# Kernel optimization log

Measured on AMD Instinct MI355X. Metric: run time of the kernel, lower is better.

The kernel has to match this reference:

```python
import jax, jax.numpy as jnp
import numpy as np

B, T, H, N, D, L, V = 4, 1024, 4, 4096, 256, 6, 256
Dh = N // H  # per-head dim; RoPE max_pos == Dh so T <= Dh
EPS = 1e-5


def _ln(x):
    # LayerNorm over last dim, no affine, eps=1e-5 (torch default)
    m = jnp.mean(x, axis=-1, keepdims=True)
    v = jnp.mean((x - m) ** 2, axis=-1, keepdims=True)
    return (x - m) / jnp.sqrt(v + EPS)


def _rope_tables(seq_len, head_dim):
    inv_freq = 1.0 / (10000.0 ** (jnp.arange(0, head_dim, 2, dtype=jnp.float32) / head_dim))
    t = jnp.arange(seq_len, dtype=jnp.float32)
    freqs = jnp.outer(t, inv_freq)            # [T, Dh/2]
    emb = jnp.concatenate([freqs, freqs], -1)  # [T, Dh]
    return jnp.cos(emb), jnp.sin(emb)


def _rotate_half(x):
    d = x.shape[-1]
    return jnp.concatenate([-x[..., d // 2:], x[..., :d // 2]], axis=-1)


def setup_inputs() -> dict:
    key = jax.random.key(0)
    ks = jax.random.split(key, 6)
    tokens = jax.random.randint(ks[0], (B, T), 0, V)
    emb_w = 0.02 * jax.random.normal(ks[1], (V, D), dtype=jnp.float32)
    E = 0.02 * jax.random.normal(ks[2], (N, D), dtype=jnp.float32)
    Dx = 0.02 * jax.random.normal(ks[3], (H, D, Dh), dtype=jnp.float32)
    Dy = 0.02 * jax.random.normal(ks[4], (H, D, Dh), dtype=jnp.float32)
    readout = 0.02 * jax.random.normal(ks[5], (D, V), dtype=jnp.float32)
    return {"tokens": tokens, "emb_w": emb_w, "E": E, "Dx": Dx, "Dy": Dy, "readout": readout}


def reference(tokens, emb_w, E, Dx, Dy, readout):
    b, t = tokens.shape
    dh = Dx.shape[-1]
    cos, sin = _rope_tables(t, dh)  # [T, Dh], broadcast over B,H
    v = _ln(emb_w[tokens])          # [B, T, D]
    for _ in range(L):
        x = jax.nn.relu(jnp.einsum('btd,hde->bhte', v, Dx))       # [B,H,T,Dh]
        xr = x * cos + _rotate_half(x) * sin                       # RoPE (Q and K share)
        scores = jnp.einsum('bhte,bhse->bhts', xr, xr)             # [B,H,T,T] (no softmax)
        a = jnp.einsum('bhts,bsd->bhtd', scores, v)                # [B,H,T,D]
        y = jax.nn.relu(jnp.einsum('bhtd,hde->bhte', a, Dy)) * x   # [B,H,T,Dh]
        y = jnp.transpose(y, (0, 2, 1, 3)).reshape(b, t, -1)       # [B,T,N]
        v = _ln(v + _ln(y @ E))
    return v @ readout  # [B,T,V]
```

## Files before the change

kernel.cpp:

```cpp
#include <hip/hip_runtime.h>
#include <cstdint>

namespace {

typedef _Float16 f16_t;
typedef _Float16 f16x8 __attribute__((ext_vector_type(8)));
typedef float    f32x4 __attribute__((ext_vector_type(4)));
typedef float    f32x16 __attribute__((ext_vector_type(16)));

constexpr int Bc = 4, Tc = 1024, Hc = 4, Dc = 256, DHc = 1024, Lc = 6, Vc = 256;
constexpr int HALFc = 512;
constexpr float EPS = 1e-5f;
constexpr long long T4q  = (long long)Tc * 4096;
constexpr long long TDq  = (long long)Tc * Dc;
constexpr long long HDDq = (long long)DHc * Dc;
constexpr long long TBUFq = (long long)Bc * Tc * Dc;

__device__ __forceinline__ int pe_perm(int v) {
  return (v & ~1023) | ((v & 511) << 1) | ((v >> 9) & 1);
}

__device__ __forceinline__ void gload16(const void* g, void* l) {
  __builtin_amdgcn_global_load_lds((const __attribute__((address_space(1))) void*)g,
                                   (__attribute__((address_space(3))) void*)l, 16, 0, 0);
}


template<int NW>
__device__ __forceinline__ void stage_kmaj(const f16_t* __restrict__ P, int k0,
                                           int ld, int c0, f16_t* S, int tid) {
  const int cg  = tid & 15;
  const int kpb = tid >> 4;
  constexpr int NP = (NW == 4) ? 2 : 1;
  #pragma unroll
  for (int p = 0; p < NP; ++p) {
    const int kp = p * 16 + kpb;
    const int k  = kp * 2;
    const f16x8 r0 = *(const f16x8*)(P + (size_t)(k0 + k) * ld + c0 + cg * 8);
    const f16x8 r1 = *(const f16x8*)(P + (size_t)(k0 + k + 1) * ld + c0 + cg * 8);
    #pragma unroll
    for (int j = 0; j < 8; ++j) {
      const int n = cg * 8 + j;
      union { f16_t h[2]; unsigned int u; } pk;
      pk.h[0] = r0[j]; pk.h[1] = r1[j];
      ((unsigned int*)S)[n * 32 + ((((kp >> 2) ^ (n & 7) ^ ((n >> 3) & 7)) & 7) << 2)
                         + (kp & 3)] = pk.u;
    }
  }
}

template<int EPI, bool AKMAJ, bool BKMAJ, int NW>
__global__ __launch_bounds__(NW * 64)
void gemm_f16(const f16_t* __restrict__ A, long long sAb, long long sAh,
              const f16_t* __restrict__ B, long long sBb, long long sBh,
              void* __restrict__ Cv, long long sCb, long long sCh,
              const f16_t* __restrict__ aux,
              int K, int lda, int ldb, int ldc,
              const float* __restrict__ cosP, const float* __restrict__ sinP)
{
  constexpr int FN2  = (NW == 4) ? 2 : 1;
  constexpr int WCW  = FN2 * 32;
  constexpr int NTHR = NW * 64;
  constexpr int SP   = 1024 / NTHR;
  constexpr int RPP  = NTHR / 8;

  __shared__ __align__(16) f16_t As[128 * 64];
  __shared__ __align__(16) f16_t Bs[128 * 64];

  const int zb = blockIdx.z >> 2, zh = blockIdx.z & 3;
  A += zb * sAb + zh * sAh;
  B += zb * sBb + zh * sBh;
  const long long Coff = zb * sCb + zh * sCh;

  const int tid  = threadIdx.x;
  const int lane = tid & 63;
  const int wave = tid >> 6;
  const int wr = (NW == 4) ? (wave >> 1) : (wave >> 2);
  const int wc = (NW == 4) ? (wave & 1)  : (wave & 3);
  const int m0 = blockIdx.y * 128, n0 = blockIdx.x * 128;

  const int lrow  = tid >> 3;
  const int lslot = tid & 7;

  f32x16 acc[2][FN2] = {};

  for (int k0 = 0; k0 < K; k0 += 64) {
    if (!AKMAJ) {
      #pragma unroll
      for (int c = 0; c < SP; ++c) {
        const int row  = c * RPP + lrow;
        const int scol = ((lslot ^ (row & 7) ^ ((row >> 3) & 7)) << 3);
        gload16(A + (size_t)(m0 + row) * lda + k0 + scol, &As[(c * NTHR + tid) * 8]);
      }
    } else {
      stage_kmaj<NW>(A, k0, lda, m0, As, tid);
    }
    if (!BKMAJ) {
      #pragma unroll
      for (int c = 0; c < SP; ++c) {
        const int row  = c * RPP + lrow;
        const int scol = ((lslot ^ (row & 7) ^ ((row >> 3) & 7)) << 3);
        gload16(B + (size_t)(n0 + row) * ldb + k0 + scol, &Bs[(c * NTHR + tid) * 8]);
      }
    } else {
      stage_kmaj<NW>(B, k0, ldb, n0, Bs, tid);
    }
    __syncthreads();

    #pragma unroll
    for (int kc = 0; kc < 4; ++kc) {
      f16x8 af[2], bf[FN2];
      #pragma unroll
      for (int m = 0; m < 2; ++m) {
        const int r  = wr * 64 + m * 32 + (lane & 31);
        const int sl = (kc * 2 + (lane >> 5)) ^ (r & 7) ^ ((r >> 3) & 7);
        af[m] = *(const f16x8*)(&As[r * 64 + sl * 8]);
      }
      #pragma unroll
      for (int n = 0; n < FN2; ++n) {
        const int r  = wc * WCW + n * 32 + (lane & 31);
        const int sl = (kc * 2 + (lane >> 5)) ^ (r & 7) ^ ((r >> 3) & 7);
        bf[n] = *(const f16x8*)(&Bs[r * 64 + sl * 8]);
      }
      #pragma unroll
      for (int m = 0; m < 2; ++m)
        #pragma unroll
        for (int n = 0; n < FN2; ++n)
          acc[m][n] = __builtin_amdgcn_mfma_f32_32x32x16_f16(af[m], bf[n], acc[m][n], 0, 0, 0);
    }
    __syncthreads();
  }

  const int rbase = 4 * (lane >> 5);
  if (EPI == 4) {
    float* C = (float*)Cv + Coff;
    #pragma unroll
    for (int m = 0; m < 2; ++m)
      #pragma unroll
      for (int n = 0; n < FN2; ++n) {
        const int gcol = n0 + wc * WCW + n * 32 + (lane & 31);
        #pragma unroll
        for (int reg = 0; reg < 16; ++reg) {
          const int grow = m0 + wr * 64 + m * 32 + (reg & 3) + 8 * (reg >> 2) + rbase;
          C[(long long)grow * ldc + gcol] = acc[m][n][reg];
        }
      }
  } else if (EPI == 5) {
    f16_t* C = (f16_t*)Cv + Coff;
    #pragma unroll
    for (int m = 0; m < 2; ++m)
      #pragma unroll
      for (int n = 0; n < FN2; ++n) {
        const int gcol = n0 + wc * WCW + n * 32 + (lane & 31);
        const int jj   = (gcol & 1023) >> 1;
        const float sg = (gcol & 1) ? 1.0f : -1.0f;
        #pragma unroll
        for (int reg = 0; reg < 16; ++reg) {
          const int grow = m0 + wr * 64 + m * 32 + (reg & 3) + 8 * (reg >> 2) + rbase;
          const int tt   = grow & (Tc - 1);
          const float val  = fmaxf(acc[m][n][reg], 0.0f);
          const float part = __shfl_xor(val, 1);
          const float c = cosP[tt * HALFc + jj];
          const float s = sinP[tt * HALFc + jj];
          C[(long long)grow * ldc + gcol] = (f16_t)(val * c + part * s * sg);
        }
      }
  } else if (EPI == 2) {
    f16_t* C = (f16_t*)Cv + Coff;
    const f16_t* X = aux + Coff;
    #pragma unroll
    for (int m = 0; m < 2; ++m)
      #pragma unroll
      for (int n = 0; n < FN2; ++n) {
        const int gcol = n0 + wc * WCW + n * 32 + (lane & 31);
        const int jj   = (gcol & 1023) >> 1;
        const float sg = (gcol & 1) ? 1.0f : -1.0f;
        #pragma unroll
        for (int reg = 0; reg < 16; ++reg) {
          const int grow = m0 + wr * 64 + m * 32 + (reg & 3) + 8 * (reg >> 2) + rbase;
          const int tt   = grow & (Tc - 1);
          const long long off = (long long)grow * ldc + gcol;
          const float xrv  = (float)X[off];
          const float part = __shfl_xor(xrv, 1);
          const float c = cosP[tt * HALFc + jj];
          const float s = sinP[tt * HALFc + jj];
          const float xv = xrv * c - part * s * sg;
          C[off] = (f16_t)(fmaxf(acc[m][n][reg], 0.0f) * xv);
        }
      }
  } else {
    f16_t* C = (f16_t*)Cv + Coff;
    #pragma unroll
    for (int m = 0; m < 2; ++m)
      #pragma unroll
      for (int n = 0; n < FN2; ++n) {
        const int gcol = n0 + wc * WCW + n * 32 + (lane & 31);
        #pragma unroll
        for (int reg = 0; reg < 16; ++reg) {
          const int grow = m0 + wr * 64 + m * 32 + (reg & 3) + 8 * (reg >> 2) + rbase;
          C[(long long)grow * ldc + gcol] = (f16_t)acc[m][n][reg];
        }
      }
  }
}

__global__ __launch_bounds__(256)
void transpose_f32_f16(const float* __restrict__ in, f16_t* __restrict__ out,
                       int R, int C, long long sIn, long long sOut,
                       int permR, int permC)
{
  __shared__ float tile[32][33];
  in  += (long long)blockIdx.z * sIn;
  out += (long long)blockIdx.z * sOut;
  const int c0 = blockIdx.x * 32, r0 = blockIdx.y * 32;
  const int tx = threadIdx.x & 31, ty = threadIdx.x >> 5;
  #pragma unroll
  for (int i = 0; i < 32; i += 8)
    tile[ty + i][tx] = in[(long long)(r0 + ty + i) * C + (c0 + tx)];
  __syncthreads();
  #pragma unroll
  for (int i = 0; i < 32; i += 8) {
    int ro = c0 + ty + i;
    int co = r0 + tx;
    if (permR) ro = pe_perm(ro);
    if (permC) co = pe_perm(co);
    out[(long long)ro * R + co] = (f16_t)tile[tx][ty + i];
  }
}

__global__ __launch_bounds__(256)
void init_tables(float* __restrict__ cosT, float* __restrict__ sinT)
{
  const int i = blockIdx.x * 256 + threadIdx.x;
  const int j = i & (HALFc - 1);
  const int t = i >> 9;
  const float inv = expf(-(float)j * (9.210340371976184f / 512.0f));
  const float ang = (float)t * inv;
  cosT[i] = cosf(ang);
  sinT[i] = sinf(ang);
}

__device__ __forceinline__ void block_stats(float val, float* red, float& mean, float& inv_std)
{
  float s1 = val, s2 = val * val;
  #pragma unroll
  for (int o = 1; o < 64; o <<= 1) {
    s1 += __shfl_xor(s1, o);
    s2 += __shfl_xor(s2, o);
  }
  const int lane = threadIdx.x & 63;
  const int w = threadIdx.x >> 6;
  if (lane == 0) { red[w * 2] = s1; red[w * 2 + 1] = s2; }
  __syncthreads();
  s1 = red[0] + red[2] + red[4] + red[6];
  s2 = red[1] + red[3] + red[5] + red[7];
  mean = s1 * (1.0f / Dc);
  const float var = s2 * (1.0f / Dc) - mean * mean;
  inv_std = 1.0f / sqrtf(var + EPS);
  __syncthreads();
}

__global__ __launch_bounds__(256)
void embed_ln(const int* __restrict__ tokens, const float* __restrict__ emb,
              f16_t* __restrict__ v)
{
  __shared__ float red[8];
  const int row = blockIdx.x;
  const int d = threadIdx.x;
  const float val = emb[(long long)tokens[row] * Dc + d];
  float m, is;
  block_stats(val, red, m, is);
  v[(long long)row * Dc + d] = (f16_t)((val - m) * is);
}

__global__ __launch_bounds__(256)
void fuse_ln4(f16_t* __restrict__ v, const float* __restrict__ t)
{
  __shared__ float red[8];
  const long long row = blockIdx.x;
  const int d = threadIdx.x;
  const long long off = row * Dc + d;
  const float tv = t[off] + t[off + TBUFq] + t[off + 2 * TBUFq] + t[off + 3 * TBUFq];
  float m1, is1;
  block_stats(tv, red, m1, is1);
  const float u = (tv - m1) * is1;
  const float wv = (float)v[off] + u;
  float m2, is2;
  block_stats(wv, red, m2, is2);
  v[off] = (f16_t)((wv - m2) * is2);
}

}

extern "C" void kernel_launch(void* const* d_in, const int* in_sizes, int n_in,
                              void* d_out, int out_size, void* d_ws, size_t ws_size,
                              hipStream_t stream)
{
  (void)in_sizes; (void)n_in; (void)out_size; (void)ws_size;
  const int*   tokens  = (const int*)d_in[0];
  const float* emb_w   = (const float*)d_in[1];
  const float* E       = (const float*)d_in[2];
  const float* Dx      = (const float*)d_in[3];
  const float* Dy      = (const float*)d_in[4];
  const float* readout = (const float*)d_in[5];
  float* out = (float*)d_out;

  char* w = (char*)d_ws;
  auto carve = [&](size_t bytes) { char* p = w; w += (bytes + 255) & ~(size_t)255; return p; };
  float* cosT = (float*)carve((size_t)Tc * HALFc * 4);
  float* sinT = (float*)carve((size_t)Tc * HALFc * 4);
  f16_t* v    = (f16_t*)carve((size_t)Bc * Tc * Dc * 2);
  f16_t* xr   = (f16_t*)carve((size_t)Bc * Tc * 4096 * 2);
  f16_t* yb   = (f16_t*)carve((size_t)Bc * Tc * 4096 * 2);
  f16_t* WT   = (f16_t*)carve((size_t)Bc * Dc * 4096 * 2);
  f16_t* a    = (f16_t*)carve((size_t)Bc * Tc * Hc * Dc * 2);
  float* t    = (float*)carve((size_t)4 * TBUFq * 4);
  f16_t* DxT  = (f16_t*)carve((size_t)Hc * DHc * Dc * 2);
  f16_t* DyT  = (f16_t*)carve((size_t)Hc * DHc * Dc * 2);
  f16_t* ET   = (f16_t*)carve((size_t)Dc * Hc * DHc * 2);
  f16_t* RT   = (f16_t*)carve((size_t)Vc * Dc * 2);

  transpose_f32_f16<<<dim3(32, 8, Hc), 256, 0, stream>>>(Dx, DxT, Dc, DHc, HDDq, HDDq, 1, 0);
  transpose_f32_f16<<<dim3(32, 8, Hc), 256, 0, stream>>>(Dy, DyT, Dc, DHc, HDDq, HDDq, 1, 0);
  transpose_f32_f16<<<dim3(8, 128, 1), 256, 0, stream>>>(E, ET, 4096, Dc, 0, 0, 0, 1);
  transpose_f32_f16<<<dim3(8, 8, 1), 256, 0, stream>>>(readout, RT, Dc, Vc, 0, 0, 0, 0);
  init_tables<<<(Tc * HALFc) / 256, 256, 0, stream>>>(cosT, sinT);
  embed_ln<<<Bc * Tc, 256, 0, stream>>>(tokens, emb_w, v);

  for (int l = 0; l < Lc; ++l) {
    gemm_f16<5, false, false, 4><<<dim3(32, 32, 1), 256, 0, stream>>>(
        v, 0, 0, DxT, 0, 0, xr, 0, 0, nullptr, Dc, Dc, Dc, 4096, cosT, sinT);
    gemm_f16<0, true, true, 8><<<dim3(32, 2, 4), 512, 0, stream>>>(
        v, 0, TDq, xr, 0, T4q, WT, 0, (long long)Dc * 4096, nullptr,
        Tc, Dc, 4096, 4096, nullptr, nullptr);
    gemm_f16<0, false, false, 8><<<dim3(2, 8, 16), 512, 0, stream>>>(
        xr, T4q, DHc, WT, (long long)Dc * 4096, DHc, a, (long long)Tc * 1024, Dc,
        nullptr, DHc, 4096, 4096, 1024, nullptr, nullptr);
    gemm_f16<2, false, false, 4><<<dim3(8, 32, 4), 256, 0, stream>>>(
        a, 0, Dc, DyT, 0, HDDq, yb, 0, DHc, xr, Dc, 1024, Dc, 4096, cosT, sinT);
    gemm_f16<4, false, false, 8><<<dim3(2, 32, 4), 512, 0, stream>>>(
        yb, 0, DHc, ET, 0, DHc, t, 0, TBUFq, nullptr, DHc, 4096, 4096, Dc,
        nullptr, nullptr);
    fuse_ln4<<<Bc * Tc, 256, 0, stream>>>(v, t);
  }

  gemm_f16<4, false, false, 8><<<dim3(2, 32, 1), 512, 0, stream>>>(
      v, 0, 0, RT, 0, 0, out, 0, 0, nullptr, Dc, Dc, Dc, Vc, nullptr, nullptr);
}
```

Measured before the change: 787.4 us.

## Store xr and yb transposed and vectorize epilogue stores along rows

The RoPE epilogue (EPI 5) and the gated epilogue (EPI 2) now write xr and yb in a column-major (feature-major) layout, with each lane storing four consecutive rows as one f16x4 vector instead of sixteen scalar strided stores. The downstream GEMMs switch their transpose template flags and strides to consume this transposed layout. The aim is to coalesce the epilogue writes and reads and to drop a B-operand transpose in the W^T GEMM. The cost is that the consuming GEMMs now load A operands in k-major form, and the buffers are resized to 4096x4096.

Result: slower. 890.2 us (+13.1%).

```diff
diff --git a/kernel.cpp b/kernel.cpp
--- a/kernel.cpp
+++ b/kernel.cpp
@@ -5,15 +5,17 @@
 
 typedef _Float16 f16_t;
 typedef _Float16 f16x8 __attribute__((ext_vector_type(8)));
+typedef _Float16 f16x4 __attribute__((ext_vector_type(4)));
 typedef float    f32x4 __attribute__((ext_vector_type(4)));
 typedef float    f32x16 __attribute__((ext_vector_type(16)));
 
 constexpr int Bc = 4, Tc = 1024, Hc = 4, Dc = 256, DHc = 1024, Lc = 6, Vc = 256;
 constexpr int HALFc = 512;
 constexpr float EPS = 1e-5f;
-constexpr long long T4q  = (long long)Tc * 4096;
-constexpr long long TDq  = (long long)Tc * Dc;
-constexpr long long HDDq = (long long)DHc * Dc;
+constexpr long long T4q   = (long long)Tc * 4096;
+constexpr long long TDq   = (long long)Tc * Dc;
+constexpr long long HDDq  = (long long)DHc * Dc;
+constexpr long long HRTq  = (long long)DHc * 4096;
 constexpr long long TBUFq = (long long)Bc * Tc * Dc;
 
 __device__ __forceinline__ int pe_perm(int v) {
@@ -146,7 +148,7 @@
         }
       }
   } else if (EPI == 5) {
-    f16_t* C = (f16_t*)Cv + Coff;
+    f16_t* C = (f16_t*)Cv;
     #pragma unroll
     for (int m = 0; m < 2; ++m)
       #pragma unroll
@@ -154,20 +156,25 @@
         const int gcol = n0 + wc * WCW + n * 32 + (lane & 31);
         const int jj   = (gcol & 1023) >> 1;
         const float sg = (gcol & 1) ? 1.0f : -1.0f;
-        #pragma unroll
-        for (int reg = 0; reg < 16; ++reg) {
-          const int grow = m0 + wr * 64 + m * 32 + (reg & 3) + 8 * (reg >> 2) + rbase;
-          const int tt   = grow & (Tc - 1);
-          const float val  = fmaxf(acc[m][n][reg], 0.0f);
-          const float part = __shfl_xor(val, 1);
-          const float c = cosP[tt * HALFc + jj];
-          const float s = sinP[tt * HALFc + jj];
-          C[(long long)grow * ldc + gcol] = (f16_t)(val * c + part * s * sg);
+        const long long cb = Coff + (long long)gcol * ldc;
+        #pragma unroll
+        for (int q = 0; q < 4; ++q) {
+          const int grow0 = m0 + wr * 64 + m * 32 + 8 * q + rbase;
+          f16x4 o;
+          #pragma unroll
+          for (int j = 0; j < 4; ++j) {
+            const float val  = fmaxf(acc[m][n][4 * q + j], 0.0f);
+            const float part = __shfl_xor(val, 1);
+            const int   tt   = (grow0 + j) & (Tc - 1);
+            const float c = cosP[tt * HALFc + jj];
+            const float s = sinP[tt * HALFc + jj];
+            o[j] = (f16_t)(val * c + part * s * sg);
+          }
+          *(f16x4*)(C + cb + grow0) = o;
         }
       }
   } else if (EPI == 2) {
-    f16_t* C = (f16_t*)Cv + Coff;
-    const f16_t* X = aux + Coff;
+    f16_t* C = (f16_t*)Cv;
     #pragma unroll
     for (int m = 0; m < 2; ++m)
       #pragma unroll
@@ -175,17 +182,23 @@
         const int gcol = n0 + wc * WCW + n * 32 + (lane & 31);
         const int jj   = (gcol & 1023) >> 1;
         const float sg = (gcol & 1) ? 1.0f : -1.0f;
-        #pragma unroll
-        for (int reg = 0; reg < 16; ++reg) {
-          const int grow = m0 + wr * 64 + m * 32 + (reg & 3) + 8 * (reg >> 2) + rbase;
-          const int tt   = grow & (Tc - 1);
-          const long long off = (long long)grow * ldc + gcol;
-          const float xrv  = (float)X[off];
-          const float part = __shfl_xor(xrv, 1);
-          const float c = cosP[tt * HALFc + jj];
-          const float s = sinP[tt * HALFc + jj];
-          const float xv = xrv * c - part * s * sg;
-          C[off] = (f16_t)(fmaxf(acc[m][n][reg], 0.0f) * xv);
+        const long long cb = Coff + (long long)gcol * ldc;
+        #pragma unroll
+        for (int q = 0; q < 4; ++q) {
+          const int grow0 = m0 + wr * 64 + m * 32 + 8 * q + rbase;
+          const f16x4 x4 = *(const f16x4*)(aux + cb + grow0);
+          f16x4 o;
+          #pragma unroll
+          for (int j = 0; j < 4; ++j) {
+            const float xrv  = (float)x4[j];
+            const float part = __shfl_xor(xrv, 1);
+            const int   tt   = (grow0 + j) & (Tc - 1);
+            const float c = cosP[tt * HALFc + jj];
+            const float s = sinP[tt * HALFc + jj];
+            const float xv = xrv * c - part * s * sg;
+            o[j] = (f16_t)(fmaxf(acc[m][n][4 * q + j], 0.0f) * xv);
+          }
+          *(f16x4*)(C + cb + grow0) = o;
         }
       }
   } else {
@@ -310,8 +323,8 @@
   float* cosT = (float*)carve((size_t)Tc * HALFc * 4);
   float* sinT = (float*)carve((size_t)Tc * HALFc * 4);
   f16_t* v    = (f16_t*)carve((size_t)Bc * Tc * Dc * 2);
-  f16_t* xr   = (f16_t*)carve((size_t)Bc * Tc * 4096 * 2);
-  f16_t* yb   = (f16_t*)carve((size_t)Bc * Tc * 4096 * 2);
+  f16_t* xr   = (f16_t*)carve((size_t)4096 * 4096 * 2);
+  f16_t* yb   = (f16_t*)carve((size_t)4096 * 4096 * 2);
   f16_t* WT   = (f16_t*)carve((size_t)Bc * Dc * 4096 * 2);
   f16_t* a    = (f16_t*)carve((size_t)Bc * Tc * Hc * Dc * 2);
   float* t    = (float*)carve((size_t)4 * TBUFq * 4);
@@ -330,16 +343,16 @@
   for (int l = 0; l < Lc; ++l) {
     gemm_f16<5, false, false, 4><<<dim3(32, 32, 1), 256, 0, stream>>>(
         v, 0, 0, DxT, 0, 0, xr, 0, 0, nullptr, Dc, Dc, Dc, 4096, cosT, sinT);
-    gemm_f16<0, true, true, 8><<<dim3(32, 2, 4), 512, 0, stream>>>(
-        v, 0, TDq, xr, 0, T4q, WT, 0, (long long)Dc * 4096, nullptr,
+    gemm_f16<0, true, false, 8><<<dim3(32, 2, 4), 512, 0, stream>>>(
+        v, 0, TDq, xr, 0, Tc, WT, 0, (long long)Dc * 4096, nullptr,
         Tc, Dc, 4096, 4096, nullptr, nullptr);
-    gemm_f16<0, false, false, 8><<<dim3(2, 8, 16), 512, 0, stream>>>(
-        xr, T4q, DHc, WT, (long long)Dc * 4096, DHc, a, (long long)Tc * 1024, Dc,
+    gemm_f16<0, true, false, 8><<<dim3(2, 8, 16), 512, 0, stream>>>(
+        xr, Tc, HRTq, WT, (long long)Dc * 4096, DHc, a, (long long)Tc * 1024, Dc,
         nullptr, DHc, 4096, 4096, 1024, nullptr, nullptr);
     gemm_f16<2, false, false, 4><<<dim3(8, 32, 4), 256, 0, stream>>>(
-        a, 0, Dc, DyT, 0, HDDq, yb, 0, DHc, xr, Dc, 1024, Dc, 4096, cosT, sinT);
-    gemm_f16<4, false, false, 8><<<dim3(2, 32, 4), 512, 0, stream>>>(
-        yb, 0, DHc, ET, 0, DHc, t, 0, TBUFq, nullptr, DHc, 4096, 4096, Dc,
+        a, 0, Dc, DyT, 0, HDDq, yb, 0, HRTq, xr, Dc, 1024, Dc, 4096, cosT, sinT);
+    gemm_f16<4, true, false, 8><<<dim3(2, 32, 4), 512, 0, stream>>>(
+        yb, 0, HRTq, ET, 0, DHc, t, 0, TBUFq, nullptr, DHc, 4096, 4096, Dc,
         nullptr, nullptr);
     fuse_ln4<<<Bc * Tc, 256, 0, stream>>>(v, t);
   }
```
